# Performance work log

Hardware: AMD Instinct MI355X
Metric: run time of the kernel (lower is better)

Reference implementation:

```python
import jax, jax.numpy as jnp
import numpy as np

B, N, H = 32, 2048, 256          # batch, num_docs, hidden_dim
F_HEADS = 8                      # config.dynamic_fusion_heads
NH = 8                           # num_heads inside each nn.MultiheadAttention
STEPS = 3                        # config.meta_adaptation_steps


def setup_inputs() -> dict:
    key = jax.random.key(0)
    ks = jax.random.split(key, 10)
    s = 0.02
    return {
        "query": jax.random.normal(ks[0], (B, H), jnp.float32),
        "retrieved_docs": jax.random.normal(ks[1], (B, N, H), jnp.float32),
        "causal_weights": jax.random.uniform(ks[2], (B, N, 1), jnp.float32),
        "context_history": jax.random.normal(ks[3], (B, H), jnp.float32),
        # per-fusion-head MultiheadAttention params (torch layout: in_proj [3H,H])
        "in_proj_w": jax.random.normal(ks[4], (F_HEADS, 3 * H, H), jnp.float32) * s,
        "in_proj_b": jnp.zeros((F_HEADS, 3 * H), jnp.float32),
        "out_proj_w": jax.random.normal(ks[5], (F_HEADS, H, H), jnp.float32) * s,
        "out_proj_b": jnp.zeros((F_HEADS, H), jnp.float32),
        "strategy_w": jax.random.normal(ks[6], (F_HEADS, H), jnp.float32) * s,
        "strategy_b": jnp.zeros((F_HEADS,), jnp.float32),
        "meta_params": jax.random.normal(ks[7], (STEPS, H, H), jnp.float32) * 0.02,
    }


def _mha_qlen1(q, kv, Wi, bi, Wo, bo):
    # q: [B,H] (query length 1), kv: [B,N,H]. Torch MHA semantics, batch_first.
    Wq, Wk, Wv = jnp.split(Wi, 3, axis=0)
    bq, bk, bv = jnp.split(bi, 3)
    dh = H // NH
    qh = (q @ Wq.T + bq).reshape(B, NH, dh)
    kh = (kv @ Wk.T + bk).reshape(B, N, NH, dh)
    vh = (kv @ Wv.T + bv).reshape(B, N, NH, dh)
    scores = jnp.einsum('bhd,bnhd->bhn', qh, kh) / jnp.sqrt(jnp.float32(dh))
    attn = jax.nn.softmax(scores, axis=-1)
    ctx = jnp.einsum('bhn,bnhd->bhd', attn, vh).reshape(B, H)
    return ctx @ Wo.T + bo


def reference(query, retrieved_docs, causal_weights, context_history,
              in_proj_w, in_proj_b, out_proj_w, out_proj_b,
              strategy_w, strategy_b, meta_params):
    # causal weighting of retrieved docs (shared across all fusion heads)
    weighted_docs = retrieved_docs * causal_weights  # [B,N,H]

    # batch all 8 fusion heads' cross-attention in one vmapped pass -> [F,B,H]
    heads_out = jax.vmap(
        lambda Wi, bi, Wo, bo: _mha_qlen1(query, weighted_docs, Wi, bi, Wo, bo)
    )(in_proj_w, in_proj_b, out_proj_w, out_proj_b)

    # sequential residual meta-adaptation steps (same matrices for every head)
    for i in range(STEPS):
        heads_out = heads_out + heads_out @ meta_params[i]

    # strategy-weighted combine of fusion heads
    strategy = jax.nn.softmax(query @ strategy_w.T + strategy_b, axis=-1)  # [B,F]
    return jnp.einsum('fbh,bf->bh', heads_out, strategy)  # [B,H]
```

## Files before the change

kernel.cpp:

```cpp
#include <hip/hip_runtime.h>
#include <hip/hip_bf16.h>


#define B_ 32
#define N_ 2048
#define H_ 256
#define F_ 8
#define FH_ 64
#define NCH_ 8

typedef unsigned short u16;
typedef __attribute__((ext_vector_type(8))) short bf16x8;
typedef __attribute__((ext_vector_type(4))) float f32x4;
#define MFMA(a, b, c) __builtin_amdgcn_mfma_f32_16x16x32_bf16((a), (b), (c), 0, 0, 0)

__device__ __forceinline__ u16 f2b(float x) {
  unsigned u = __builtin_bit_cast(unsigned, x);
  return (u16)((u + 0x7fffu + ((u >> 16) & 1u)) >> 16);
}
__device__ __forceinline__ float b2f(u16 h) {
  unsigned u = ((unsigned)h) << 16;
  return __builtin_bit_cast(float, u);
}

static constexpr size_t UB_U     = 0;
static constexpr size_t UB_W     = 1048576;
static constexpr size_t UB_PM    = 3145728;
static constexpr size_t UB_PL    = 3276800;
static constexpr size_t UB_STRAT = 3424256;
static constexpr size_t UB_HO    = 3425280;

__global__ __launch_bounds__(512) void k1_mfma(
    const float* __restrict__ query, const float* __restrict__ ipw,
    const float* __restrict__ ipb, const float* __restrict__ stw,
    const float* __restrict__ stb, u16* __restrict__ u, float* __restrict__ strat)
{
  const int f = blockIdx.x >> 1, hf = blockIdx.x & 1;
  const int tid = threadIdx.x, L = tid & 63, w = tid >> 6;
  const int khi = L >> 4, col = L & 15;

  __shared__ u16 sW[256 * 40];
  __shared__ u16 qhh[32 * 136];
  __shared__ u16 qhl[32 * 136];
  __shared__ float slog[256];

  bf16x8 qf[2][8];
  #pragma unroll
  for (int bt = 0; bt < 2; ++bt)
    #pragma unroll
    for (int ks = 0; ks < 8; ++ks) {
      const float* qp = &query[(size_t)(bt * 16 + col) * H_ + ks * 32 + khi * 8];
      float4 v0 = *(const float4*)qp, v1 = *(const float4*)(qp + 4);
      bf16x8 q;
      q[0] = f2b(v0.x); q[1] = f2b(v0.y); q[2] = f2b(v0.z); q[3] = f2b(v0.w);
      q[4] = f2b(v1.x); q[5] = f2b(v1.y); q[6] = f2b(v1.z); q[7] = f2b(v1.w);
      qf[bt][ks] = q;
    }

  if (f == 0 && hf == 0 && w == 0) {
    f32x4 sacc[2] = {(f32x4){0.f,0.f,0.f,0.f}, (f32x4){0.f,0.f,0.f,0.f}};
    #pragma unroll
    for (int ks = 0; ks < 8; ++ks) {
      bf16x8 a = (bf16x8){0,0,0,0,0,0,0,0};
      if (col < 8) {
        const float* sp = &stw[(size_t)col * H_ + ks * 32 + khi * 8];
        float4 v0 = *(const float4*)sp, v1 = *(const float4*)(sp + 4);
        a[0] = f2b(v0.x); a[1] = f2b(v0.y); a[2] = f2b(v0.z); a[3] = f2b(v0.w);
        a[4] = f2b(v1.x); a[5] = f2b(v1.y); a[6] = f2b(v1.z); a[7] = f2b(v1.w);
      }
      sacc[0] = MFMA(a, qf[0][ks], sacc[0]);
      sacc[1] = MFMA(a, qf[1][ks], sacc[1]);
    }
    if (khi < 2) {
      #pragma unroll
      for (int bt = 0; bt < 2; ++bt)
        #pragma unroll
        for (int r = 0; r < 4; ++r) {
          int i = khi * 4 + r;
          slog[(bt * 16 + col) * 8 + i] = sacc[bt][r] + stb[i];
        }
    }
  }

  f32x4 qacc[2] = {(f32x4){0.f,0.f,0.f,0.f}, (f32x4){0.f,0.f,0.f,0.f}};
  for (int ks = 0; ks < 8; ++ks) {
    #pragma unroll
    for (int p = 0; p < 2; ++p) {
      int gid = tid + 512 * p;
      int r = gid >> 3, kq = (gid & 7) * 4;
      float4 v = *(const float4*)&ipw[((size_t)(f * 768) + hf * 128 + r) * H_ + ks * 32 + kq];
      *(ushort4*)&sW[r * 40 + kq] = make_ushort4(f2b(v.x), f2b(v.y), f2b(v.z), f2b(v.w));
    }
    __syncthreads();
    bf16x8 a = *(const bf16x8*)&sW[(w * 16 + col) * 40 + khi * 8];
    qacc[0] = MFMA(a, qf[0][ks], qacc[0]);
    qacc[1] = MFMA(a, qf[1][ks], qacc[1]);
    __syncthreads();
  }
  {
    int r0 = w * 16 + khi * 4;
    float4 bq = *(const float4*)&ipb[f * 768 + hf * 128 + r0];
    #pragma unroll
    for (int bt = 0; bt < 2; ++bt) {
      int b = bt * 16 + col;
      float v0 = qacc[bt][0] + bq.x, v1 = qacc[bt][1] + bq.y;
      float v2 = qacc[bt][2] + bq.z, v3 = qacc[bt][3] + bq.w;
      ushort4 hs = make_ushort4(f2b(v0), f2b(v1), f2b(v2), f2b(v3));
      ushort4 ls = make_ushort4(f2b(v0 - b2f(hs.x)), f2b(v1 - b2f(hs.y)),
                                f2b(v2 - b2f(hs.z)), f2b(v3 - b2f(hs.w)));
      *(ushort4*)&qhh[b * 136 + r0] = hs;
      *(ushort4*)&qhl[b * 136 + r0] = ls;
    }
  }
  __syncthreads();

  if (f == 0 && hf == 0 && tid < 32) {
    float mx = slog[tid * 8];
    #pragma unroll
    for (int i = 1; i < F_; ++i) mx = fmaxf(mx, slog[tid * 8 + i]);
    float s = 0.f, e[F_];
    #pragma unroll
    for (int i = 0; i < F_; ++i) { e[i] = __expf(slog[tid * 8 + i] - mx); s += e[i]; }
    #pragma unroll
    for (int i = 0; i < F_; ++i) strat[tid * F_ + i] = e[i] / s;
  }

  const float scale = 0.17677669529663687f;
  for (int hh = 0; hh < 4; ++hh) {
    #pragma unroll
    for (int p = 0; p < 4; ++p) {
      int gid = tid + 512 * p;
      int d = gid >> 6, jq = (gid & 63) * 4;
      float4 v = *(const float4*)&ipw[((size_t)(f * 768 + 256) + (hf * 4 + hh) * 32 + d) * H_ + jq];
      float vv[4] = {v.x, v.y, v.z, v.w};
      #pragma unroll
      for (int e = 0; e < 4; ++e) {
        int j = jq + e;
        sW[j * 40 + (d ^ (((j >> 4) & 3) << 3))] = f2b(vv[e]);
      }
    }
    __syncthreads();
    #pragma unroll
    for (int q = 0; q < 2; ++q) {
      int jt = w * 2 + q;
      bf16x8 a = *(const bf16x8*)&sW[(jt * 16 + col) * 40 + ((khi ^ (jt & 3)) * 8)];
      #pragma unroll
      for (int bt = 0; bt < 2; ++bt) {
        int b = bt * 16 + col;
        bf16x8 bh = *(const bf16x8*)&qhh[b * 136 + hh * 32 + khi * 8];
        bf16x8 bl = *(const bf16x8*)&qhl[b * 136 + hh * 32 + khi * 8];
        f32x4 acc = (f32x4){0.f, 0.f, 0.f, 0.f};
        acc = MFMA(a, bh, acc);
        acc = MFMA(a, bl, acc);
        int j0 = jt * 16 + khi * 4;
        ushort4 us = make_ushort4(f2b(acc[0] * scale), f2b(acc[1] * scale),
                                  f2b(acc[2] * scale), f2b(acc[3] * scale));
        *(ushort4*)&u[((size_t)(b * 64) + f * 8 + hf * 4 + hh) * H_ + j0] = us;
      }
    }
    __syncthreads();
  }
}

__global__ __launch_bounds__(512) void k2_stats(
    const float* __restrict__ docs, const float* __restrict__ cw,
    const u16* __restrict__ u, float* __restrict__ pm, float* __restrict__ pl)
{
  const int ns = blockIdx.x, b = blockIdx.y;
  const int n0 = ns * 256;
  const int tid = threadIdx.x, L = tid & 63, w = tid >> 6;
  const int khi = L >> 4, col = L & 15;

  __shared__ u16 sdu[256 * 72];
  __shared__ bf16x8 su8[64 * 9];
  __shared__ float scw[256];
  __shared__ float swred[8][64];
  __shared__ float sbm[64];

  if (tid < 256) scw[tid] = cw[b * N_ + n0 + tid];

  f32x4 acc[2][4];
  #pragma unroll
  for (int t = 0; t < 2; ++t)
    #pragma unroll
    for (int nt = 0; nt < 4; ++nt) acc[t][nt] = (f32x4){0.f, 0.f, 0.f, 0.f};

  float4 dv[8];
  #pragma unroll
  for (int p = 0; p < 8; ++p) {
    int idx = tid + 512 * p;
    int n = idx >> 4, jq = (idx & 15) * 4;
    dv[p] = *(const float4*)&docs[((size_t)(b * N_) + n0 + n) * H_ + jq];
  }

  for (int jv = 0; jv < 4; ++jv) {
    const int j0 = jv * 64;
    if (jv) __syncthreads();
    {
      int fh = tid >> 3, sub = tid & 7;
      su8[fh * 9 + sub] = *(const bf16x8*)&u[((size_t)(b * 64) + fh) * H_ + j0 + sub * 8];
    }
    #pragma unroll
    for (int p = 0; p < 8; ++p) {
      int idx = tid + 512 * p;
      int n = idx >> 4, jq = (idx & 15) * 4;
      *(ushort4*)&sdu[n * 72 + jq] =
          make_ushort4(f2b(dv[p].x), f2b(dv[p].y), f2b(dv[p].z), f2b(dv[p].w));
    }
    if (jv < 3) {
      #pragma unroll
      for (int p = 0; p < 8; ++p) {
        int idx = tid + 512 * p;
        int n = idx >> 4, jq = (idx & 15) * 4;
        dv[p] = *(const float4*)&docs[((size_t)(b * N_) + n0 + n) * H_ + j0 + 64 + jq];
      }
    }
    __syncthreads();
    #pragma unroll
    for (int kk = 0; kk < 64; kk += 32) {
      bf16x8 a0 = *(const bf16x8*)&sdu[(w * 32 + col) * 72 + kk + khi * 8];
      bf16x8 a1 = *(const bf16x8*)&sdu[(w * 32 + 16 + col) * 72 + kk + khi * 8];
      #pragma unroll
      for (int nt = 0; nt < 4; ++nt) {
        bf16x8 bb = su8[(nt * 16 + col) * 9 + kk / 8 + khi];
        acc[0][nt] = MFMA(a0, bb, acc[0][nt]);
        acc[1][nt] = MFMA(a1, bb, acc[1][nt]);
      }
    }
  }
  float cwv[2][4];
  #pragma unroll
  for (int t = 0; t < 2; ++t)
    #pragma unroll
    for (int r = 0; r < 4; ++r) cwv[t][r] = scw[w * 32 + t * 16 + khi * 4 + r];

  float mx[4];
  #pragma unroll
  for (int nt = 0; nt < 4; ++nt) {
    mx[nt] = -3.4e38f;
    #pragma unroll
    for (int t = 0; t < 2; ++t)
      #pragma unroll
      for (int r = 0; r < 4; ++r) {
        float sv = acc[t][nt][r] * cwv[t][r];
        acc[t][nt][r] = sv;
        mx[nt] = fmaxf(mx[nt], sv);
      }
    mx[nt] = fmaxf(mx[nt], __shfl_xor(mx[nt], 16, 64));
    mx[nt] = fmaxf(mx[nt], __shfl_xor(mx[nt], 32, 64));
  }
  if (L < 16) {
    #pragma unroll
    for (int nt = 0; nt < 4; ++nt) swred[w][nt * 16 + L] = mx[nt];
  }
  __syncthreads();
  if (tid < 64) {
    float m = swred[0][tid];
    #pragma unroll
    for (int ww = 1; ww < 8; ++ww) m = fmaxf(m, swred[ww][tid]);
    sbm[tid] = m;
  }
  __syncthreads();
  float ls[4];
  #pragma unroll
  for (int nt = 0; nt < 4; ++nt) {
    float bm = sbm[nt * 16 + col];
    ls[nt] = 0.f;
    #pragma unroll
    for (int t = 0; t < 2; ++t)
      #pragma unroll
      for (int r = 0; r < 4; ++r) ls[nt] += __expf(acc[t][nt][r] - bm);
    ls[nt] += __shfl_xor(ls[nt], 16, 64);
    ls[nt] += __shfl_xor(ls[nt], 32, 64);
  }
  __syncthreads();
  if (L < 16) {
    #pragma unroll
    for (int nt = 0; nt < 4; ++nt) swred[w][nt * 16 + L] = ls[nt];
  }
  __syncthreads();
  if (tid < 64) {
    float bl = 0.f;
    #pragma unroll
    for (int ww = 0; ww < 8; ++ww) bl += swred[ww][tid];
    size_t ro = (size_t)(b * 64 + tid) * NCH_ + ns;
    pm[ro] = sbm[tid];
    pl[ro] = bl;
  }
}

__global__ __launch_bounds__(512) void k4_part(
    const float* __restrict__ docs, const float* __restrict__ cw,
    const u16* __restrict__ u, const float* __restrict__ pm,
    const float* __restrict__ pl, float* __restrict__ wbuf)
{
  const int ns = blockIdx.x, b = blockIdx.y;
  const int n0 = ns * 256;
  const int tid = threadIdx.x, L = tid & 63, w = tid >> 6;
  const int khi = L >> 4, col = L & 15;
  const int ft = w & 3, nt0 = (w >> 2) * 2;

  __shared__ u16 sdu[64 * 264];
  __shared__ u16 phu[64 * 72];
  __shared__ u16 plou[64 * 72];
  __shared__ float sm_l[64], sl_l[64];

  if (tid < 64) {
    size_t ro = (size_t)(b * 64 + tid) * NCH_;
    float m = pm[ro];
    for (int cc = 1; cc < NCH_; ++cc) m = fmaxf(m, pm[ro + cc]);
    float l = 0.f;
    for (int cc = 0; cc < NCH_; ++cc) l += pl[ro + cc] * __expf(pm[ro + cc] - m);
    sm_l[tid] = m;
    sl_l[tid] = 1.f / l;
  }

  bf16x8 uf[8];
  #pragma unroll
  for (int ks = 0; ks < 8; ++ks)
    uf[ks] = *(const bf16x8*)&u[((size_t)(b * 64) + ft * 16 + col) * H_ + ks * 32 + khi * 8];

  float4 dv[8];
  #pragma unroll
  for (int p = 0; p < 8; ++p) {
    int idx = tid + 512 * p;
    int n = idx >> 6, jq = (idx & 63) * 4;
    dv[p] = *(const float4*)&docs[((size_t)(b * N_) + n0 + n) * H_ + jq];
  }
  #pragma unroll
  for (int p = 0; p < 8; ++p) {
    int idx = tid + 512 * p;
    int n = idx >> 6, jq = (idx & 63) * 4;
    *(ushort4*)&sdu[n * 264 + (jq ^ (((n >> 3) & 3) << 4))] =
        make_ushort4(f2b(dv[p].x), f2b(dv[p].y), f2b(dv[p].z), f2b(dv[p].w));
  }
  __syncthreads();

  f32x4 acc2[4][2];
  #pragma unroll
  for (int mt = 0; mt < 4; ++mt)
    #pragma unroll
    for (int jt = 0; jt < 2; ++jt) acc2[mt][jt] = (f32x4){0.f, 0.f, 0.f, 0.f};

  for (int nc = 0; nc < 4; ++nc) {
    if (nc < 3) {
      #pragma unroll
      for (int p = 0; p < 8; ++p) {
        int idx = tid + 512 * p;
        int n = idx >> 6, jq = (idx & 63) * 4;
        dv[p] = *(const float4*)&docs[((size_t)(b * N_) + n0 + (nc + 1) * 64 + n) * H_ + jq];
      }
    }
    f32x4 sc0 = (f32x4){0.f, 0.f, 0.f, 0.f}, sc1 = sc0;
    const int nr0 = nt0 * 16 + col, nr1 = (nt0 + 1) * 16 + col;
    const int sw0 = ((nr0 >> 3) & 3) << 4, sw1 = ((nr1 >> 3) & 3) << 4;
    #pragma unroll
    for (int ks = 0; ks < 8; ++ks) {
      bf16x8 b0 = *(const bf16x8*)&sdu[nr0 * 264 + ((ks * 32 + khi * 8) ^ sw0)];
      bf16x8 b1 = *(const bf16x8*)&sdu[nr1 * 264 + ((ks * 32 + khi * 8) ^ sw1)];
      sc0 = MFMA(uf[ks], b0, sc0);
      sc1 = MFMA(uf[ks], b1, sc1);
    }
    {
      int ng = n0 + nc * 64 + nt0 * 16 + col;
      float cv0 = cw[(size_t)b * N_ + ng];
      float cv1 = cw[(size_t)b * N_ + ng + 16];
      #pragma unroll
      for (int r = 0; r < 4; ++r) {
        int fh = ft * 16 + khi * 4 + r;
        float m = sm_l[fh], li = sl_l[fh];
        float p0 = __expf(sc0[r] * cv0 - m) * li * cv0;
        float p1 = __expf(sc1[r] * cv1 - m) * li * cv1;
        u16 h0 = f2b(p0), h1 = f2b(p1);
        phu [fh * 72 + nt0 * 16 + col]       = h0;
        plou[fh * 72 + nt0 * 16 + col]       = f2b(p0 - b2f(h0));
        phu [fh * 72 + (nt0 + 1) * 16 + col] = h1;
        plou[fh * 72 + (nt0 + 1) * 16 + col] = f2b(p1 - b2f(h1));
      }
    }
    __syncthreads();

    #pragma unroll
    for (int kk = 0; kk < 2; ++kk) {
      #pragma unroll
      for (int jt = 0; jt < 2; ++jt) {
        int j = w * 32 + jt * 16 + col;
        bf16x8 bb;
        #pragma unroll
        for (int jj = 0; jj < 8; ++jj)
          bb[jj] = (short)sdu[(kk * 32 + khi * 8 + jj) * 264 + (j ^ (khi << 4))];
        #pragma unroll
        for (int mt = 0; mt < 4; ++mt) {
          bf16x8 ah = *(const bf16x8*)&phu [(mt * 16 + col) * 72 + kk * 32 + khi * 8];
          bf16x8 al = *(const bf16x8*)&plou[(mt * 16 + col) * 72 + kk * 32 + khi * 8];
          acc2[mt][jt] = MFMA(ah, bb, acc2[mt][jt]);
          acc2[mt][jt] = MFMA(al, bb, acc2[mt][jt]);
        }
      }
    }
    __syncthreads();

    if (nc < 3) {
      #pragma unroll
      for (int p = 0; p < 8; ++p) {
        int idx = tid + 512 * p;
        int n = idx >> 6, jq = (idx & 63) * 4;
        *(ushort4*)&sdu[n * 264 + (jq ^ (((n >> 3) & 3) << 4))] =
            make_ushort4(f2b(dv[p].x), f2b(dv[p].y), f2b(dv[p].z), f2b(dv[p].w));
      }
      __syncthreads();
    }
  }
  #pragma unroll
  for (int mt = 0; mt < 4; ++mt)
    #pragma unroll
    for (int jt = 0; jt < 2; ++jt)
      #pragma unroll
      for (int r = 0; r < 4; ++r) {
        int fh = mt * 16 + khi * 4 + r;
        int j = w * 32 + jt * 16 + col;
        atomicAdd(&wbuf[((size_t)(b * 64) + fh) * H_ + j], acc2[mt][jt][r]);
      }
}

__global__ __launch_bounds__(256) void kt_meta(
    const float* __restrict__ meta, u16* __restrict__ metaT)
{
  const int s = blockIdx.x, xg = blockIdx.y;
  const int x0 = xg * 32;
  const int tid = threadIdx.x;
  __shared__ u16 sT[32 * 264];
  #pragma unroll
  for (int p = 0; p < 8; ++p) {
    int idx = tid + 256 * p;
    int r = idx >> 3, xq = (idx & 7) * 4;
    float4 v = *(const float4*)&meta[((size_t)(s * 256) + r) * 256 + x0 + xq];
    sT[(xq + 0) * 264 + r] = f2b(v.x);
    sT[(xq + 1) * 264 + r] = f2b(v.y);
    sT[(xq + 2) * 264 + r] = f2b(v.z);
    sT[(xq + 3) * 264 + r] = f2b(v.w);
  }
  __syncthreads();
  #pragma unroll
  for (int p = 0; p < 4; ++p) {
    int idx = tid + 256 * p;
    int x = idx >> 5, rq = (idx & 31) * 8;
    bf16x8 v = *(bf16x8*)&sT[x * 264 + rq];
    *(bf16x8*)&metaT[((size_t)(s * 256) + x0 + x) * 256 + rq] = v;
  }
}

__global__ __launch_bounds__(512) void k5_mfma(
    const float* __restrict__ ipw, const float* __restrict__ ipb,
    const float* __restrict__ opw, const float* __restrict__ opb,
    const u16* __restrict__ metaT, const float* __restrict__ wbuf,
    float* __restrict__ ho)
{
  const int f = blockIdx.x & 7, b0 = (blockIdx.x >> 3) * 16;
  const int tid = threadIdx.x, L = tid & 63, w = tid >> 6;
  const int khi = L >> 4, col = L & 15;

  __shared__ char smem[57856];
  u16* sWvP  = (u16*)(smem);
  u16* sWhiP = (u16*)(smem + 20480);
  u16* sWloP = (u16*)(smem + 30720);
  u16* sWo   = (u16*)(smem);
  u16* XBh   = (u16*)(smem + 20480);
  u16* XBl   = (u16*)(smem + 28928);
  u16* XAh   = (u16*)(smem + 40960);
  u16* XAl   = (u16*)(smem + 49408);

  f32x4 cacc0 = (f32x4){0.f, 0.f, 0.f, 0.f};
  f32x4 cacc1 = (f32x4){0.f, 0.f, 0.f, 0.f};
  for (int ks = 0; ks < 8; ++ks) {
    #pragma unroll
    for (int p = 0; p < 4; ++p) {
      int idx = tid + 512 * p;
      int r = idx >> 3, cq = (idx & 7) * 4;
      float4 v = *(const float4*)&ipw[((size_t)(f * 768 + 512) + r) * 256 + ks * 32 + cq];
      *(ushort4*)&sWvP[r * 40 + cq] = make_ushort4(f2b(v.x), f2b(v.y), f2b(v.z), f2b(v.w));
    }
    #pragma unroll
    for (int p = 0; p < 2; ++p) {
      int idx = tid + 512 * p;
      int rr = idx >> 3, cq = (idx & 7) * 4;
      int h = rr >> 4, b = rr & 15;
      float4 v = *(const float4*)&wbuf[((size_t)((b0 + b) * 64) + f * 8 + h) * 256 + ks * 32 + cq];
      u16 hx = f2b(v.x), hy = f2b(v.y), hz = f2b(v.z), hw2 = f2b(v.w);
      *(ushort4*)&sWhiP[rr * 40 + cq] = make_ushort4(hx, hy, hz, hw2);
      *(ushort4*)&sWloP[rr * 40 + cq] = make_ushort4(
          f2b(v.x - b2f(hx)), f2b(v.y - b2f(hy)), f2b(v.z - b2f(hz)), f2b(v.w - b2f(hw2)));
    }
    __syncthreads();
    bf16x8 bh = *(bf16x8*)&sWhiP[(w * 16 + col) * 40 + khi * 8];
    bf16x8 bl = *(bf16x8*)&sWloP[(w * 16 + col) * 40 + khi * 8];
    bf16x8 a0 = *(bf16x8*)&sWvP[(w * 32 + col) * 40 + khi * 8];
    bf16x8 a1 = *(bf16x8*)&sWvP[(w * 32 + 16 + col) * 40 + khi * 8];
    cacc0 = MFMA(a0, bh, cacc0); cacc0 = MFMA(a0, bl, cacc0);
    cacc1 = MFMA(a1, bh, cacc1); cacc1 = MFMA(a1, bl, cacc1);
    __syncthreads();
  }
  #pragma unroll
  for (int mt = 0; mt < 2; ++mt) {
    f32x4 cv = mt ? cacc1 : cacc0;
    #pragma unroll
    for (int r = 0; r < 4; ++r) {
      int d = mt * 16 + khi * 4 + r;
      float vv = cv[r] + ipb[f * 768 + 512 + w * 32 + d];
      u16 hi = f2b(vv);
      XAh[col * 264 + w * 32 + d] = hi;
      XAl[col * 264 + w * 32 + d] = f2b(vv - b2f(hi));
    }
  }

  f32x4 hr0, hr1;
  {
    float bo0 = opb[f * 256 + (w * 2 + 0) * 16 + col];
    float bo1 = opb[f * 256 + (w * 2 + 1) * 16 + col];
    hr0 = (f32x4){bo0, bo0, bo0, bo0};
    hr1 = (f32x4){bo1, bo1, bo1, bo1};
  }
  for (int ks = 0; ks < 8; ++ks) {
    #pragma unroll
    for (int p = 0; p < 4; ++p) {
      int idx = tid + 512 * p;
      int r = idx >> 3, cq = (idx & 7) * 4;
      float4 v = *(const float4*)&opw[((size_t)(f * 256) + r) * 256 + ks * 32 + cq];
      *(ushort4*)&sWo[r * 40 + cq] = make_ushort4(f2b(v.x), f2b(v.y), f2b(v.z), f2b(v.w));
    }
    __syncthreads();
    bf16x8 ah  = *(bf16x8*)&XAh[col * 264 + ks * 32 + khi * 8];
    bf16x8 al  = *(bf16x8*)&XAl[col * 264 + ks * 32 + khi * 8];
    bf16x8 bw0 = *(bf16x8*)&sWo[((w * 2 + 0) * 16 + col) * 40 + khi * 8];
    bf16x8 bw1 = *(bf16x8*)&sWo[((w * 2 + 1) * 16 + col) * 40 + khi * 8];
    hr0 = MFMA(ah, bw0, hr0); hr0 = MFMA(al, bw0, hr0);
    hr1 = MFMA(ah, bw1, hr1); hr1 = MFMA(al, bw1, hr1);
    __syncthreads();
  }

  auto spill = [&](u16* Oh, u16* Ol) {
    #pragma unroll
    for (int q = 0; q < 2; ++q) {
      f32x4 hv = q ? hr1 : hr0;
      int x = (w * 2 + q) * 16 + col;
      #pragma unroll
      for (int r = 0; r < 4; ++r) {
        u16 hi = f2b(hv[r]);
        Oh[(khi * 4 + r) * 264 + x] = hi;
        Ol[(khi * 4 + r) * 264 + x] = f2b(hv[r] - b2f(hi));
      }
    }
  };
  auto meta_mm = [&](const u16* Ah_, const u16* Al_, int s) {
    f32x4 n0 = hr0, n1 = hr1;
    #pragma unroll
    for (int ks = 0; ks < 8; ++ks) {
      bf16x8 ah = *(const bf16x8*)&Ah_[col * 264 + ks * 32 + khi * 8];
      bf16x8 al = *(const bf16x8*)&Al_[col * 264 + ks * 32 + khi * 8];
      const u16* mrow = &metaT[((size_t)(s * 256) + (w * 2) * 16 + col) * 256 + ks * 32 + khi * 8];
      bf16x8 m0 = *(const bf16x8*)mrow;
      bf16x8 m1 = *(const bf16x8*)(mrow + 16 * 256);
      n0 = MFMA(ah, m0, n0); n0 = MFMA(al, m0, n0);
      n1 = MFMA(ah, m1, n1); n1 = MFMA(al, m1, n1);
    }
    hr0 = n0; hr1 = n1;
  };

  spill(XBh, XBl);
  __syncthreads();
  meta_mm(XBh, XBl, 0);
  spill(XAh, XAl);
  __syncthreads();
  meta_mm(XAh, XAl, 1);
  spill(XBh, XBl);
  __syncthreads();
  meta_mm(XBh, XBl, 2);

  #pragma unroll
  for (int q = 0; q < 2; ++q) {
    f32x4 hv = q ? hr1 : hr0;
    int x = (w * 2 + q) * 16 + col;
    #pragma unroll
    for (int r = 0; r < 4; ++r) {
      int b = khi * 4 + r;
      ho[((size_t)(f * B_) + b0 + b) * 256 + x] = hv[r];
    }
  }
}

__global__ __launch_bounds__(256) void k6_combine(
    const float* __restrict__ ho, const float* __restrict__ strat,
    float* __restrict__ out)
{
  const int b = blockIdx.x;
  const int tid = threadIdx.x;
  float acc = 0.f;
  #pragma unroll
  for (int f = 0; f < F_; ++f)
    acc += strat[b * F_ + f] * ho[((size_t)(f * B_) + b) * H_ + tid];
  out[b * H_ + tid] = acc;
}

extern "C" void kernel_launch(void* const* d_in, const int* in_sizes, int n_in,
                              void* d_out, int out_size, void* d_ws, size_t ws_size,
                              hipStream_t stream) {
  const float* query = (const float*)d_in[0];
  const float* docs  = (const float*)d_in[1];
  const float* cw    = (const float*)d_in[2];
  const float* ipw   = (const float*)d_in[4];
  const float* ipb   = (const float*)d_in[5];
  const float* opw   = (const float*)d_in[6];
  const float* opb   = (const float*)d_in[7];
  const float* stw   = (const float*)d_in[8];
  const float* stb   = (const float*)d_in[9];
  const float* meta  = (const float*)d_in[10];
  float* out = (float*)d_out;

  char* base = (char*)d_ws;
  u16*   u     = (u16*)(base + UB_U);
  u16*   metaT = (u16*)(base + UB_U);
  float* wbuf  = (float*)(base + UB_W);
  float* pm    = (float*)(base + UB_PM);
  float* pl    = (float*)(base + UB_PL);
  float* strat = (float*)(base + UB_STRAT);
  float* ho    = (float*)(base + UB_HO);

  hipMemsetAsync(wbuf, 0, (size_t)B_ * FH_ * H_ * sizeof(float), stream);
  k1_mfma<<<dim3(16), 512, 0, stream>>>(query, ipw, ipb, stw, stb, u, strat);
  k2_stats<<<dim3(NCH_, B_), 512, 0, stream>>>(docs, cw, u, pm, pl);
  k4_part<<<dim3(NCH_, B_), 512, 0, stream>>>(docs, cw, u, pm, pl, wbuf);
  kt_meta<<<dim3(3, 8), 256, 0, stream>>>(meta, metaT);
  k5_mfma<<<dim3(16), 512, 0, stream>>>(ipw, ipb, opw, opb, metaT, wbuf, ho);
  k6_combine<<<dim3(B_), 256, 0, stream>>>(ho, strat, out);
}
```

Before: 209.1 us.

## Drop softmax stats pass, use unnormalized exp with deferred normalization

```diff
diff --git a/kernel.cpp b/kernel.cpp
--- a/kernel.cpp
+++ b/kernel.cpp
@@ -25,20 +25,45 @@
 
 static constexpr size_t UB_U     = 0;
 static constexpr size_t UB_W     = 1048576;
-static constexpr size_t UB_PM    = 3145728;
-static constexpr size_t UB_PL    = 3276800;
-static constexpr size_t UB_STRAT = 3424256;
-static constexpr size_t UB_HO    = 3425280;
-
-__global__ __launch_bounds__(512) void k1_mfma(
+static constexpr size_t UB_L     = 3145728;
+static constexpr size_t UB_STRAT = 3153920;
+static constexpr size_t UB_MT    = 3154944;
+
+__global__ __launch_bounds__(512) void k1_fused(
     const float* __restrict__ query, const float* __restrict__ ipw,
     const float* __restrict__ ipb, const float* __restrict__ stw,
-    const float* __restrict__ stb, u16* __restrict__ u, float* __restrict__ strat)
+    const float* __restrict__ stb, const float* __restrict__ meta,
+    u16* __restrict__ u, u16* __restrict__ metaT, float* __restrict__ strat)
 {
-  const int f = blockIdx.x >> 1, hf = blockIdx.x & 1;
   const int tid = threadIdx.x, L = tid & 63, w = tid >> 6;
   const int khi = L >> 4, col = L & 15;
 
+  if (blockIdx.x >= 16) {
+    const int bid2 = blockIdx.x - 16;
+    const int s = bid2 >> 3, x0 = (bid2 & 7) * 32;
+    __shared__ u16 sT[32 * 264];
+    #pragma unroll
+    for (int p = 0; p < 4; ++p) {
+      int idx = tid + 512 * p;
+      int r = idx >> 3, xq = (idx & 7) * 4;
+      float4 v = *(const float4*)&meta[((size_t)(s * 256) + r) * 256 + x0 + xq];
+      sT[(xq + 0) * 264 + r] = f2b(v.x);
+      sT[(xq + 1) * 264 + r] = f2b(v.y);
+      sT[(xq + 2) * 264 + r] = f2b(v.z);
+      sT[(xq + 3) * 264 + r] = f2b(v.w);
+    }
+    __syncthreads();
+    #pragma unroll
+    for (int p = 0; p < 2; ++p) {
+      int idx = tid + 512 * p;
+      int x = idx >> 5, rq = (idx & 31) * 8;
+      bf16x8 v = *(bf16x8*)&sT[x * 264 + rq];
+      *(bf16x8*)&metaT[((size_t)(s * 256) + x0 + x) * 256 + rq] = v;
+    }
+    return;
+  }
+
+  const int f = blockIdx.x >> 1, hf = blockIdx.x & 1;
   __shared__ u16 sW[256 * 40];
   __shared__ u16 qhh[32 * 136];
   __shared__ u16 qhl[32 * 136];
@@ -162,137 +187,9 @@
   }
 }
 
-__global__ __launch_bounds__(512) void k2_stats(
+__global__ __launch_bounds__(512) void k4_one(
     const float* __restrict__ docs, const float* __restrict__ cw,
-    const u16* __restrict__ u, float* __restrict__ pm, float* __restrict__ pl)
-{
-  const int ns = blockIdx.x, b = blockIdx.y;
-  const int n0 = ns * 256;
-  const int tid = threadIdx.x, L = tid & 63, w = tid >> 6;
-  const int khi = L >> 4, col = L & 15;
-
-  __shared__ u16 sdu[256 * 72];
-  __shared__ bf16x8 su8[64 * 9];
-  __shared__ float scw[256];
-  __shared__ float swred[8][64];
-  __shared__ float sbm[64];
-
-  if (tid < 256) scw[tid] = cw[b * N_ + n0 + tid];
-
-  f32x4 acc[2][4];
-  #pragma unroll
-  for (int t = 0; t < 2; ++t)
-    #pragma unroll
-    for (int nt = 0; nt < 4; ++nt) acc[t][nt] = (f32x4){0.f, 0.f, 0.f, 0.f};
-
-  float4 dv[8];
-  #pragma unroll
-  for (int p = 0; p < 8; ++p) {
-    int idx = tid + 512 * p;
-    int n = idx >> 4, jq = (idx & 15) * 4;
-    dv[p] = *(const float4*)&docs[((size_t)(b * N_) + n0 + n) * H_ + jq];
-  }
-
-  for (int jv = 0; jv < 4; ++jv) {
-    const int j0 = jv * 64;
-    if (jv) __syncthreads();
-    {
-      int fh = tid >> 3, sub = tid & 7;
-      su8[fh * 9 + sub] = *(const bf16x8*)&u[((size_t)(b * 64) + fh) * H_ + j0 + sub * 8];
-    }
-    #pragma unroll
-    for (int p = 0; p < 8; ++p) {
-      int idx = tid + 512 * p;
-      int n = idx >> 4, jq = (idx & 15) * 4;
-      *(ushort4*)&sdu[n * 72 + jq] =
-          make_ushort4(f2b(dv[p].x), f2b(dv[p].y), f2b(dv[p].z), f2b(dv[p].w));
-    }
-    if (jv < 3) {
-      #pragma unroll
-      for (int p = 0; p < 8; ++p) {
-        int idx = tid + 512 * p;
-        int n = idx >> 4, jq = (idx & 15) * 4;
-        dv[p] = *(const float4*)&docs[((size_t)(b * N_) + n0 + n) * H_ + j0 + 64 + jq];
-      }
-    }
-    __syncthreads();
-    #pragma unroll
-    for (int kk = 0; kk < 64; kk += 32) {
-      bf16x8 a0 = *(const bf16x8*)&sdu[(w * 32 + col) * 72 + kk + khi * 8];
-      bf16x8 a1 = *(const bf16x8*)&sdu[(w * 32 + 16 + col) * 72 + kk + khi * 8];
-      #pragma unroll
-      for (int nt = 0; nt < 4; ++nt) {
-        bf16x8 bb = su8[(nt * 16 + col) * 9 + kk / 8 + khi];
-        acc[0][nt] = MFMA(a0, bb, acc[0][nt]);
-        acc[1][nt] = MFMA(a1, bb, acc[1][nt]);
-      }
-    }
-  }
-  float cwv[2][4];
-  #pragma unroll
-  for (int t = 0; t < 2; ++t)
-    #pragma unroll
-    for (int r = 0; r < 4; ++r) cwv[t][r] = scw[w * 32 + t * 16 + khi * 4 + r];
-
-  float mx[4];
-  #pragma unroll
-  for (int nt = 0; nt < 4; ++nt) {
-    mx[nt] = -3.4e38f;
-    #pragma unroll
-    for (int t = 0; t < 2; ++t)
-      #pragma unroll
-      for (int r = 0; r < 4; ++r) {
-        float sv = acc[t][nt][r] * cwv[t][r];
-        acc[t][nt][r] = sv;
-        mx[nt] = fmaxf(mx[nt], sv);
-      }
-    mx[nt] = fmaxf(mx[nt], __shfl_xor(mx[nt], 16, 64));
-    mx[nt] = fmaxf(mx[nt], __shfl_xor(mx[nt], 32, 64));
-  }
-  if (L < 16) {
-    #pragma unroll
-    for (int nt = 0; nt < 4; ++nt) swred[w][nt * 16 + L] = mx[nt];
-  }
-  __syncthreads();
-  if (tid < 64) {
-    float m = swred[0][tid];
-    #pragma unroll
-    for (int ww = 1; ww < 8; ++ww) m = fmaxf(m, swred[ww][tid]);
-    sbm[tid] = m;
-  }
-  __syncthreads();
-  float ls[4];
-  #pragma unroll
-  for (int nt = 0; nt < 4; ++nt) {
-    float bm = sbm[nt * 16 + col];
-    ls[nt] = 0.f;
-    #pragma unroll
-    for (int t = 0; t < 2; ++t)
-      #pragma unroll
-      for (int r = 0; r < 4; ++r) ls[nt] += __expf(acc[t][nt][r] - bm);
-    ls[nt] += __shfl_xor(ls[nt], 16, 64);
-    ls[nt] += __shfl_xor(ls[nt], 32, 64);
-  }
-  __syncthreads();
-  if (L < 16) {
-    #pragma unroll
-    for (int nt = 0; nt < 4; ++nt) swred[w][nt * 16 + L] = ls[nt];
-  }
-  __syncthreads();
-  if (tid < 64) {
-    float bl = 0.f;
-    #pragma unroll
-    for (int ww = 0; ww < 8; ++ww) bl += swred[ww][tid];
-    size_t ro = (size_t)(b * 64 + tid) * NCH_ + ns;
-    pm[ro] = sbm[tid];
-    pl[ro] = bl;
-  }
-}
-
-__global__ __launch_bounds__(512) void k4_part(
-    const float* __restrict__ docs, const float* __restrict__ cw,
-    const u16* __restrict__ u, const float* __restrict__ pm,
-    const float* __restrict__ pl, float* __restrict__ wbuf)
+    const u16* __restrict__ u, float* __restrict__ wbuf, float* __restrict__ lbuf)
 {
   const int ns = blockIdx.x, b = blockIdx.y;
   const int n0 = ns * 256;
@@ -303,17 +200,6 @@
   __shared__ u16 sdu[64 * 264];
   __shared__ u16 phu[64 * 72];
   __shared__ u16 plou[64 * 72];
-  __shared__ float sm_l[64], sl_l[64];
-
-  if (tid < 64) {
-    size_t ro = (size_t)(b * 64 + tid) * NCH_;
-    float m = pm[ro];
-    for (int cc = 1; cc < NCH_; ++cc) m = fmaxf(m, pm[ro + cc]);
-    float l = 0.f;
-    for (int cc = 0; cc < NCH_; ++cc) l += pl[ro + cc] * __expf(pm[ro + cc] - m);
-    sm_l[tid] = m;
-    sl_l[tid] = 1.f / l;
-  }
 
   bf16x8 uf[8];
   #pragma unroll
@@ -341,6 +227,7 @@
   for (int mt = 0; mt < 4; ++mt)
     #pragma unroll
     for (int jt = 0; jt < 2; ++jt) acc2[mt][jt] = (f32x4){0.f, 0.f, 0.f, 0.f};
+  float eacc[4] = {0.f, 0.f, 0.f, 0.f};
 
   for (int nc = 0; nc < 4; ++nc) {
     if (nc < 3) {
@@ -368,9 +255,10 @@
       #pragma unroll
       for (int r = 0; r < 4; ++r) {
         int fh = ft * 16 + khi * 4 + r;
-        float m = sm_l[fh], li = sl_l[fh];
-        float p0 = __expf(sc0[r] * cv0 - m) * li * cv0;
-        float p1 = __expf(sc1[r] * cv1 - m) * li * cv1;
+        float ex0 = __expf(sc0[r] * cv0);
+        float ex1 = __expf(sc1[r] * cv1);
+        eacc[r] += ex0 + ex1;
+        float p0 = ex0 * cv0, p1 = ex1 * cv1;
         u16 h0 = f2b(p0), h1 = f2b(p1);
         phu [fh * 72 + nt0 * 16 + col]       = h0;
         plou[fh * 72 + nt0 * 16 + col]       = f2b(p0 - b2f(h0));
@@ -421,32 +309,15 @@
         int j = w * 32 + jt * 16 + col;
         atomicAdd(&wbuf[((size_t)(b * 64) + fh) * H_ + j], acc2[mt][jt][r]);
       }
-}
-
-__global__ __launch_bounds__(256) void kt_meta(
-    const float* __restrict__ meta, u16* __restrict__ metaT)
-{
-  const int s = blockIdx.x, xg = blockIdx.y;
-  const int x0 = xg * 32;
-  const int tid = threadIdx.x;
-  __shared__ u16 sT[32 * 264];
-  #pragma unroll
-  for (int p = 0; p < 8; ++p) {
-    int idx = tid + 256 * p;
-    int r = idx >> 3, xq = (idx & 7) * 4;
-    float4 v = *(const float4*)&meta[((size_t)(s * 256) + r) * 256 + x0 + xq];
-    sT[(xq + 0) * 264 + r] = f2b(v.x);
-    sT[(xq + 1) * 264 + r] = f2b(v.y);
-    sT[(xq + 2) * 264 + r] = f2b(v.z);
-    sT[(xq + 3) * 264 + r] = f2b(v.w);
-  }
-  __syncthreads();
-  #pragma unroll
-  for (int p = 0; p < 4; ++p) {
-    int idx = tid + 256 * p;
-    int x = idx >> 5, rq = (idx & 31) * 8;
-    bf16x8 v = *(bf16x8*)&sT[x * 264 + rq];
-    *(bf16x8*)&metaT[((size_t)(s * 256) + x0 + x) * 256 + rq] = v;
+  #pragma unroll
+  for (int r = 0; r < 4; ++r) {
+    float e = eacc[r];
+    e += __shfl_xor(e, 1, 64);
+    e += __shfl_xor(e, 2, 64);
+    e += __shfl_xor(e, 4, 64);
+    e += __shfl_xor(e, 8, 64);
+    if (col == 0)
+      atomicAdd(&lbuf[(size_t)(b * 64) + ft * 16 + khi * 4 + r], e);
   }
 }
 
@@ -454,13 +325,15 @@
     const float* __restrict__ ipw, const float* __restrict__ ipb,
     const float* __restrict__ opw, const float* __restrict__ opb,
     const u16* __restrict__ metaT, const float* __restrict__ wbuf,
-    float* __restrict__ ho)
+    const float* __restrict__ lbuf, const float* __restrict__ strat,
+    float* __restrict__ out)
 {
   const int f = blockIdx.x & 7, b0 = (blockIdx.x >> 3) * 16;
   const int tid = threadIdx.x, L = tid & 63, w = tid >> 6;
   const int khi = L >> 4, col = L & 15;
 
   __shared__ char smem[57856];
+  __shared__ float sli[128];
   u16* sWvP  = (u16*)(smem);
   u16* sWhiP = (u16*)(smem + 20480);
   u16* sWloP = (u16*)(smem + 30720);
@@ -470,6 +343,10 @@
   u16* XAh   = (u16*)(smem + 40960);
   u16* XAl   = (u16*)(smem + 49408);
 
+  if (tid < 128)
+    sli[tid] = 1.f / lbuf[(size_t)((b0 + (tid & 15)) * 64) + f * 8 + (tid >> 4)];
+  __syncthreads();
+
   f32x4 cacc0 = (f32x4){0.f, 0.f, 0.f, 0.f};
   f32x4 cacc1 = (f32x4){0.f, 0.f, 0.f, 0.f};
   for (int ks = 0; ks < 8; ++ks) {
@@ -485,7 +362,9 @@
       int idx = tid + 512 * p;
       int rr = idx >> 3, cq = (idx & 7) * 4;
       int h = rr >> 4, b = rr & 15;
+      float li = sli[rr];
       float4 v = *(const float4*)&wbuf[((size_t)((b0 + b) * 64) + f * 8 + h) * 256 + ks * 32 + cq];
+      v.x *= li; v.y *= li; v.z *= li; v.w *= li;
       u16 hx = f2b(v.x), hy = f2b(v.y), hz = f2b(v.z), hw2 = f2b(v.w);
       *(ushort4*)&sWhiP[rr * 40 + cq] = make_ushort4(hx, hy, hz, hw2);
       *(ushort4*)&sWloP[rr * 40 + cq] = make_ushort4(
@@ -583,22 +462,10 @@
     #pragma unroll
     for (int r = 0; r < 4; ++r) {
       int b = khi * 4 + r;
-      ho[((size_t)(f * B_) + b0 + b) * 256 + x] = hv[r];
-    }
-  }
-}
-
-__global__ __launch_bounds__(256) void k6_combine(
-    const float* __restrict__ ho, const float* __restrict__ strat,
-    float* __restrict__ out)
-{
-  const int b = blockIdx.x;
-  const int tid = threadIdx.x;
-  float acc = 0.f;
-  #pragma unroll
-  for (int f = 0; f < F_; ++f)
-    acc += strat[b * F_ + f] * ho[((size_t)(f * B_) + b) * H_ + tid];
-  out[b * H_ + tid] = acc;
+      float sv = strat[(b0 + b) * F_ + f];
+      atomicAdd(&out[(size_t)(b0 + b) * H_ + x], sv * hv[r]);
+    }
+  }
 }
 
 extern "C" void kernel_launch(void* const* d_in, const int* in_sizes, int n_in,
@@ -618,18 +485,16 @@
 
   char* base = (char*)d_ws;
   u16*   u     = (u16*)(base + UB_U);
-  u16*   metaT = (u16*)(base + UB_U);
   float* wbuf  = (float*)(base + UB_W);
-  float* pm    = (float*)(base + UB_PM);
-  float* pl    = (float*)(base + UB_PL);
+  float* lbuf  = (float*)(base + UB_L);
   float* strat = (float*)(base + UB_STRAT);
-  float* ho    = (float*)(base + UB_HO);
-
-  hipMemsetAsync(wbuf, 0, (size_t)B_ * FH_ * H_ * sizeof(float), stream);
-  k1_mfma<<<dim3(16), 512, 0, stream>>>(query, ipw, ipb, stw, stb, u, strat);
-  k2_stats<<<dim3(NCH_, B_), 512, 0, stream>>>(docs, cw, u, pm, pl);
-  k4_part<<<dim3(NCH_, B_), 512, 0, stream>>>(docs, cw, u, pm, pl, wbuf);
-  kt_meta<<<dim3(3, 8), 256, 0, stream>>>(meta, metaT);
-  k5_mfma<<<dim3(16), 512, 0, stream>>>(ipw, ipb, opw, opb, metaT, wbuf, ho);
-  k6_combine<<<dim3(B_), 256, 0, stream>>>(ho, strat, out);
+  u16*   metaT = (u16*)(base + UB_MT);
+
+  hipMemsetAsync(out, 0, (size_t)B_ * H_ * sizeof(float), stream);
+  hipMemsetAsync(base + UB_W, 0,
+                 (size_t)(B_ * FH_ * H_ * sizeof(float) + B_ * FH_ * sizeof(float)),
+                 stream);
+  k1_fused<<<dim3(40), 512, 0, stream>>>(query, ipw, ipb, stw, stb, meta, u, metaT, strat);
+  k4_one<<<dim3(NCH_, B_), 512, 0, stream>>>(docs, cw, u, wbuf, lbuf);
+  k5_mfma<<<dim3(16), 512, 0, stream>>>(ipw, ipb, opw, opb, metaT, wbuf, lbuf, strat, out);
 }
```

Result: faster. 195.6 us (-6.5%).
